# Kernel tuning notes

Hardware: AMD Instinct MI355X
Metric: run time of the kernel (lower is better)

Reference implementation:

```python
import jax, jax.numpy as jnp
import numpy as np

N_NODES = 50000      # nodes
N_EDGES = 800000     # directed edges (avg degree 16)
HIDDEN = 128
F_IN = 11            # QM9 num_node_features
NUM_CLASSES = 19     # QM9 num targets
NUM_GRAPHS = 2048


def _glorot(key, fan_in, fan_out):
    lim = np.sqrt(6.0 / (fan_in + fan_out)).astype(np.float32)
    return jax.random.uniform(key, (fan_in, fan_out), jnp.float32, -lim, lim)


def setup_inputs() -> dict:
    key = jax.random.key(0)
    ks = jax.random.split(key, 8)
    x = jax.random.normal(ks[0], (N_NODES, F_IN), jnp.float32)
    edge_index = jax.random.randint(ks[1], (2, N_EDGES), 0, N_NODES, dtype=jnp.int64)
    batch = jnp.sort(jax.random.randint(ks[2], (N_NODES,), 0, NUM_GRAPHS, dtype=jnp.int64))
    W1 = _glorot(ks[3], F_IN, HIDDEN); b1 = jnp.zeros((HIDDEN,), jnp.float32)
    W2 = _glorot(ks[4], HIDDEN, HIDDEN); b2 = jnp.zeros((HIDDEN,), jnp.float32)
    W3 = _glorot(ks[5], HIDDEN, HIDDEN); b3 = jnp.zeros((HIDDEN,), jnp.float32)
    Wl = _glorot(ks[6], HIDDEN, NUM_CLASSES); bl = jnp.zeros((NUM_CLASSES,), jnp.float32)
    return dict(x=x, edge_index=edge_index, batch=batch,
                W1=W1, b1=b1, W2=W2, b2=b2, W3=W3, b3=b3, Wl=Wl, bl=bl)


def gcn_conv(x, src, dst, W, b, n):
    """PyG GCNConv: x' = D^-1/2 (A + I) D^-1/2 (x W) + b, degrees include self-loops."""
    h = x @ W                                                      # [n, out]
    deg = jax.ops.segment_sum(jnp.ones_like(dst, h.dtype), dst, num_segments=n) + 1.0
    dinv = jax.lax.rsqrt(deg)                                      # [n]
    norm = dinv[src] * dinv[dst]                                   # [E]
    agg = jax.ops.segment_sum(h[src] * norm[:, None], dst, num_segments=n)
    agg = agg + h * (dinv * dinv)[:, None]                         # self-loop term
    return agg + b


def reference(x, edge_index, batch, W1, b1, W2, b2, W3, b3, Wl, bl):
    src, dst = edge_index[0], edge_index[1]
    h = jax.nn.relu(gcn_conv(x, src, dst, W1, b1, N_NODES))
    h = jax.nn.relu(gcn_conv(h, src, dst, W2, b2, N_NODES))
    h = gcn_conv(h, src, dst, W3, b3, N_NODES)
    # global_mean_pool over graph ids
    sums = jax.ops.segment_sum(h, batch, num_segments=NUM_GRAPHS)
    cnt = jax.ops.segment_sum(jnp.ones((N_NODES,), h.dtype), batch, num_segments=NUM_GRAPHS)
    pooled = sums / jnp.maximum(cnt, 1.0)[:, None]                 # [G, H]
    # dropout is identity in eval mode
    return pooled @ Wl + bl                                        # [G, NUM_CLASSES]
```

## Files before the change

kernel.cpp:

```cpp
#include <hip/hip_runtime.h>
#include <hip/hip_bf16.h>
#include <hip/hip_fp16.h>


#define HIDDEN 128
#define F_IN 11
#define NCLS 19
#define NBITS 8
#define NB 256
#define RNODES 256
#define EPB 4096
#define OUTL_CAP 5376
#define WST 136

typedef _Float16 half8 __attribute__((ext_vector_type(8)));
typedef _Float16 half2v __attribute__((ext_vector_type(2)));
typedef float floatx4 __attribute__((ext_vector_type(4)));

#define MIXFMA4(A, UX, UY, DV) \
    asm("v_fma_mix_f32 %0, %4, %5, %0 op_sel_hi:[1,0,0]\n\t" \
        "v_fma_mix_f32 %1, %4, %5, %1 op_sel:[1,0,0] op_sel_hi:[1,0,0]\n\t" \
        "v_fma_mix_f32 %2, %6, %5, %2 op_sel_hi:[1,0,0]\n\t" \
        "v_fma_mix_f32 %3, %6, %5, %3 op_sel:[1,0,0] op_sel_hi:[1,0,0]" \
        : "+v"(A.x), "+v"(A.y), "+v"(A.z), "+v"(A.w) \
        : "v"(UX), "v"(DV), "v"(UY))

#define MIXFMA2(AX, AY, UU, DV) \
    asm("v_fma_mix_f32 %0, %2, %3, %0 op_sel_hi:[1,0,0]\n\t" \
        "v_fma_mix_f32 %1, %2, %3, %1 op_sel:[1,0,0] op_sel_hi:[1,0,0]" \
        : "+v"(AX), "+v"(AY) : "v"(UU), "v"(DV))

#define MIXFMA1(AX, HU, DV) \
    asm("v_fma_mix_f32 %0, %1, %2, %0 op_sel_hi:[1,0,0]" \
        : "+v"(AX) : "v"(HU), "v"(DV))

#define DOT2(ACC, UA, UB) \
    ACC = __builtin_amdgcn_fdot2(__builtin_bit_cast(half2v, UA), \
                                 __builtin_bit_cast(half2v, UB), ACC, false)


__global__ __launch_bounds__(1024) void scatter_kernel(
        const int* __restrict__ src, const int* __restrict__ dst,
        int* __restrict__ bcur, unsigned int* __restrict__ bents,
        int E, int cap, int nSB,
        const float* __restrict__ W3, const float* __restrict__ Wl,
        const float* __restrict__ b3, __half* __restrict__ W3lTh,
        float* __restrict__ b3l, const float* __restrict__ W2,
        __half* __restrict__ W2Th) {
    __shared__ int hist[NB];
    __shared__ int binoff[NB];
    __shared__ int runrel[NB];
    __shared__ unsigned int ebuf[EPB];
    __shared__ unsigned short binOf[EPB];
    __shared__ int cw[4];
    int tid = threadIdx.x, lane = tid & 63, w = tid >> 6;

    if (blockIdx.x >= nSB) {
        int xb = blockIdx.x - nSB;
        if (xb < 3) {
            float* Wls = (float*)ebuf;
            for (int i = tid; i < HIDDEN * NCLS; i += 1024) Wls[i] = Wl[i];
            __syncthreads();
            int o = xb * 1024 + tid;
            if (o < HIDDEN * NCLS) {
                int i = o / NCLS, j = o % NCLS;
                float acc = 0.f;
#pragma unroll 8
                for (int k = 0; k < HIDDEN; ++k) acc += W3[i * HIDDEN + k] * Wls[k * NCLS + j];
                W3lTh[j * WST + i] = __float2half(acc);
            }
            if (xb == 2 && tid >= 1000 && tid < 1000 + NCLS) {
                int j = tid - 1000;
                float acc = 0.f;
#pragma unroll 8
                for (int k = 0; k < HIDDEN; ++k) acc += b3[k] * Wls[k * NCLS + j];
                b3l[j] = acc;
            }
        } else {
            int base = (xb - 3) * 4096;
#pragma unroll
            for (int r = 0; r < 4; ++r) {
                int idx = base + tid + 1024 * r;
                int k = idx >> 7, nn2 = idx & 127;
                W2Th[nn2 * HIDDEN + k] = __float2half(W2[idx]);
            }
        }
        return;
    }

    int base = blockIdx.x * EPB;
    int cnt = min(EPB, E - base);
    if (tid < NB) hist[tid] = 0;
    __syncthreads();
    unsigned int pk[4];
    int rk[4];
#pragma unroll
    for (int j = 0; j < 4; ++j) {
        int idx = tid + 1024 * j;
        if (idx < cnt) {
            int e = base + idx;
            int s = src[e], d = dst[e];
            pk[j] = (unsigned int)s | ((unsigned int)d << 16);
            int bin = d >> NBITS;
            int r = atomicAdd(&hist[bin], 1);
            rk[j] = r | (bin << 16);
        } else rk[j] = -1;
    }
    __syncthreads();
    if (tid < NB) {
        int v = hist[tid], xv = v;
#pragma unroll
        for (int d = 1; d < 64; d <<= 1) {
            int t = __shfl_up(xv, d, 64);
            if (lane >= d) xv += t;
        }
        if (lane == 63) cw[w] = xv;
        binoff[tid] = xv - v;
        runrel[tid] = v ? atomicAdd(&bcur[tid], v) : 0;
    }
    __syncthreads();
    if (tid < NB) {
        int waveoff = 0;
        for (int wi = 0; wi < w; ++wi) waveoff += cw[wi];
        binoff[tid] += waveoff;
    }
    __syncthreads();
#pragma unroll
    for (int j = 0; j < 4; ++j) {
        if (rk[j] >= 0) {
            int bin = rk[j] >> 16, r = rk[j] & 0xFFFF;
            int pos = binoff[bin] + r;
            ebuf[pos] = pk[j];
            binOf[pos] = (unsigned short)bin;
        }
    }
    __syncthreads();
    for (int i = tid; i < cnt; i += 1024) {
        int bin = binOf[i];
        int rel = runrel[bin] + (i - binoff[bin]);
        if (rel < cap)
            bents[bin * cap + rel] = ebuf[i];
    }
}

__global__ __launch_bounds__(1024) void build_kernel(
        const unsigned int* __restrict__ bents, const int* __restrict__ bcur,
        const float* __restrict__ x, const int* __restrict__ batch,
        int2* __restrict__ begend, unsigned short* __restrict__ csr16,
        float* __restrict__ dinv, float* __restrict__ gcnt,
        __half* __restrict__ x16h, int n, int cap, int rst) {
    __shared__ int counts[RNODES];
    __shared__ int lcur[RNODES];
    __shared__ unsigned short outl[OUTL_CAP];
    __shared__ int wsums[4];
    int tid = threadIdx.x;
    int lane = tid & 63, w = tid >> 6;
    int b = blockIdx.x;
    int base = b << NBITS;
    int nn = min(RNODES, n - base);
    int ebase = b * cap;
    int ecnt = min(bcur[b], cap);
    int st = b * rst;
    if (tid < RNODES) counts[tid] = 0;
    __syncthreads();
    for (int e = tid; e < ecnt; e += 1024)
        atomicAdd(&counts[(bents[ebase + e] >> 16) - base], 1);
    __syncthreads();
    int v = 0, xv = 0;
    if (tid < RNODES) {
        v = (tid < nn) ? counts[tid] + 1 : 0;
        xv = v;
#pragma unroll
        for (int d = 1; d < 64; d <<= 1) {
            int t = __shfl_up(xv, d, 64);
            if (lane >= d) xv += t;
        }
        if (lane == 63) wsums[w] = xv;
    }
    __syncthreads();
    if (tid < nn) {
        int waveoff = 0;
        for (int wi = 0; wi < w; ++wi) waveoff += wsums[wi];
        int excl = waveoff + xv - v;
        lcur[tid] = excl + 1;
        outl[excl] = (unsigned short)(base + tid);
        begend[base + tid] = make_int2(st + excl, st + excl + v);
        atomicAdd(&gcnt[batch[base + tid]], 1.0f);
    }
    __syncthreads();
    for (int e = tid; e < ecnt; e += 1024) {
        unsigned int pk = bents[ebase + e];
        int i = (int)(pk >> 16) - base;
        int r = atomicAdd(&lcur[i], 1);
        outl[r] = (unsigned short)(pk & 0xFFFFu);
    }
    __syncthreads();
    int total = ecnt + nn;
    for (int i = tid; i < total; i += 1024)
        csr16[st + i] = outl[i];
    for (int idx = tid; idx < nn * 16; idx += 1024) {
        int i = idx >> 4, j = idx & 15;
        float di = 1.0f / sqrtf((float)(counts[i] + 1));
        if (j == 0) dinv[base + i] = di;
        float xv2 = (j < F_IN) ? x[(long)(base + i) * F_IN + j] * di : 0.f;
        x16h[(long)(base + i) * 16 + j] = __float2half(xv2);
    }
}


__global__ __launch_bounds__(1024) void agg16_gemm_kernel(
        const __half* __restrict__ x16h, const int2* __restrict__ begend,
        const unsigned short* __restrict__ csr16,
        const float* __restrict__ dinv, const float* __restrict__ W1,
        const float* __restrict__ b1, __half* __restrict__ h1h, int n) {
    __shared__ float2 W1s[F_IN][64];
    __shared__ float2 bs[64];
    int tid = threadIdx.x;
    if (tid < 352) ((float4*)W1s)[tid] = ((const float4*)W1)[tid];
    if (tid >= 960) bs[tid - 960] = make_float2(b1[2 * (tid - 960)], b1[2 * (tid - 960) + 1]);
    __syncthreads();
    int node = (int)(((long)blockIdx.x * blockDim.x + tid) >> 6);
    int lane = tid & 63;
    if (node >= n) return;
    int grp = lane >> 4, f = lane & 15;
    float di = dinv[node];
    int2 be = begend[node];
    int beg = be.x, end = be.y;
    int deg = end - beg;
    int idxv = (lane < deg) ? (int)csr16[beg + lane] : 0;
    int lim = (deg > 64) ? beg + 64 : end;
    const unsigned short* x16u = (const unsigned short*)x16h;
    float acc = 0.f;
    int eb = beg;
    for (; eb + 16 <= lim; eb += 16) {
        int off = eb - beg;
        int s[4]; unsigned int v[4];
#pragma unroll
        for (int j = 0; j < 4; ++j) s[j] = __shfl(idxv, off + grp + 4 * j);
#pragma unroll
        for (int j = 0; j < 4; ++j) v[j] = x16u[(long)s[j] * 16 + f];
#pragma unroll
        for (int j = 0; j < 4; ++j) MIXFMA1(acc, v[j], di);
    }
    if (eb + 8 <= lim) {
        int off = eb - beg;
        int s0 = __shfl(idxv, off + grp), s1 = __shfl(idxv, off + grp + 4);
        unsigned int v0 = x16u[(long)s0 * 16 + f], v1 = x16u[(long)s1 * 16 + f];
        MIXFMA1(acc, v0, di);
        MIXFMA1(acc, v1, di);
        eb += 8;
    }
#pragma unroll
    for (int r = 0; r < 2; ++r) {
        int e = eb + grp + 4 * r;
        int s = __shfl(idxv, (e - beg) & 63);
        if (e < lim) {
            unsigned int v = x16u[(long)s * 16 + f];
            MIXFMA1(acc, v, di);
        }
    }
    for (int e = lim + grp; e < end; e += 4) {
        unsigned int v = x16u[(long)csr16[e] * 16 + f];
        MIXFMA1(acc, v, di);
    }
    acc += __shfl_down(acc, 32);
    acc += __shfl_down(acc, 16);
    float z = acc;
    float2 o = bs[lane];
#pragma unroll
    for (int k = 0; k < F_IN; ++k) {
        float zk = __shfl(z, k);
        float2 w = W1s[k][lane];
        o.x += zk * w.x;
        o.y += zk * w.y;
    }
    __half2 h = __floats2half2_rn(fmaxf(o.x, 0.f), fmaxf(o.y, 0.f));
    ((__half2*)h1h)[(long)node * 64 + lane] = h;
}


__global__ __launch_bounds__(256) void gemm_mfma_kernel(
        const __half* __restrict__ h1h, const __half* __restrict__ W2Th,
        const float* __restrict__ dinv, __half* __restrict__ hsh, int n) {
    __shared__ _Float16 W2T[128 * 136];
    __shared__ _Float16 outs[64 * 136];
    int tid = threadIdx.x;
    for (int i = tid; i < 128 * 16; i += 256) {
        int r = i >> 4, q = i & 15;
        *(uint4*)&W2T[r * 136 + q * 8] = ((const uint4*)W2Th)[r * 16 + q];
    }
    int base = blockIdx.x * 64;
    int lane = tid & 63, wid = tid >> 6;
    int l15 = lane & 15, quad = lane >> 4;
    int arow = base + wid * 16 + l15;
    if (arow >= n) arow = n - 1;
    const _Float16* Aptr = (const _Float16*)h1h + (size_t)arow * 128;
    floatx4 acc[8];
#pragma unroll
    for (int t = 0; t < 8; ++t) acc[t] = (floatx4){0.f, 0.f, 0.f, 0.f};
    __syncthreads();
#pragma unroll
    for (int c = 0; c < 4; ++c) {
        half8 a = *(const half8*)(Aptr + c * 32 + quad * 8);
#pragma unroll
        for (int t = 0; t < 8; ++t) {
            half8 b = *(const half8*)(&W2T[(t * 16 + l15) * 136 + c * 32 + quad * 8]);
            acc[t] = __builtin_amdgcn_mfma_f32_16x16x32_f16(a, b, acc[t], 0, 0, 0);
        }
    }
    float dv[4];
#pragma unroll
    for (int r = 0; r < 4; ++r) {
        int nd = base + wid * 16 + quad * 4 + r;
        dv[r] = dinv[(nd < n) ? nd : 0];
    }
#pragma unroll
    for (int t = 0; t < 8; ++t)
#pragma unroll
        for (int r = 0; r < 4; ++r)
            outs[(wid * 16 + quad * 4 + r) * 136 + t * 16 + l15] = (_Float16)(acc[t][r] * dv[r]);
    __syncthreads();
    for (int i = tid; i < 64 * 16; i += 256) {
        int ln = i >> 4, qq = i & 15;
        long nd = base + ln;
        if (nd < n) {
            uint4 u = *(uint4*)&outs[ln * 136 + qq * 8];
            ((uint4*)hsh)[nd * 16 + qq] = u;
        }
    }
}


__global__ __launch_bounds__(1024) void agg128h_y_kernel(
        const __half* __restrict__ hsh, const int2* __restrict__ begend,
        const unsigned short* __restrict__ csr16, const float* __restrict__ dinv,
        const float* __restrict__ bias, const __half* __restrict__ W3lTh,
        __half* __restrict__ ys, int n) {
    __shared__ _Float16 Ws[32 * WST];
    __shared__ _Float16 hs[16][HIDDEN];
    int tid = threadIdx.x;
    if (tid < 544) ((float4*)Ws)[tid] = ((const float4*)W3lTh)[tid];
    __syncthreads();
    int node = (int)(((long)blockIdx.x * blockDim.x + tid) >> 6);
    if (node >= n) return;
    int lane = tid & 63, w = tid >> 6;
    int grp = lane >> 5, q = lane & 31;
    float di = dinv[node];
    int2 be = begend[node];
    int beg = be.x, end = be.y;
    int deg = end - beg;
    int idxv = (lane < deg) ? (int)csr16[beg + lane] : 0;
    int lim = (deg > 64) ? beg + 64 : end;
    float4 acc = make_float4(0.f, 0.f, 0.f, 0.f);
    int eb = beg;
    for (; eb + 16 <= lim; eb += 16) {
        int off = eb - beg;
        int s[8]; uint2 u[8];
#pragma unroll
        for (int j = 0; j < 8; ++j) s[j] = __shfl(idxv, off + grp + 2 * j);
#pragma unroll
        for (int j = 0; j < 8; ++j) u[j] = ((const uint2*)hsh)[(long)s[j] * 32 + q];
#pragma unroll
        for (int j = 0; j < 8; ++j) MIXFMA4(acc, u[j].x, u[j].y, di);
    }
    if (eb + 8 <= lim) {
        int off = eb - beg;
        int s[4]; uint2 u[4];
#pragma unroll
        for (int j = 0; j < 4; ++j) s[j] = __shfl(idxv, off + grp + 2 * j);
#pragma unroll
        for (int j = 0; j < 4; ++j) u[j] = ((const uint2*)hsh)[(long)s[j] * 32 + q];
#pragma unroll
        for (int j = 0; j < 4; ++j) MIXFMA4(acc, u[j].x, u[j].y, di);
        eb += 8;
    }
#pragma unroll
    for (int r = 0; r < 4; ++r) {
        int e = eb + grp + 2 * r;
        int s = __shfl(idxv, (e - beg) & 63);
        if (e < lim) {
            uint2 u = ((const uint2*)hsh)[(long)s * 32 + q];
            MIXFMA4(acc, u.x, u.y, di);
        }
    }
    for (int e = lim + grp; e < end; e += 2) {
        uint2 u = ((const uint2*)hsh)[(long)csr16[e] * 32 + q];
        MIXFMA4(acc, u.x, u.y, di);
    }
    acc.x += __shfl_down(acc.x, 32);
    acc.y += __shfl_down(acc.y, 32);
    acc.z += __shfl_down(acc.z, 32);
    acc.w += __shfl_down(acc.w, 32);
    if (grp == 0) {
        float4 b = ((const float4*)bias)[q];
        __half2 p01 = __floats2half2_rn(fmaxf(acc.x + b.x, 0.f), fmaxf(acc.y + b.y, 0.f));
        __half2 p23 = __floats2half2_rn(fmaxf(acc.z + b.z, 0.f), fmaxf(acc.w + b.w, 0.f));
        uint2 hv = make_uint2(*(unsigned int*)&p01, *(unsigned int*)&p23);
        *(uint2*)&hs[w][q * 4] = hv;
    }
    asm volatile("s_waitcnt lgkmcnt(0)" ::: "memory");
    float yacc = 0.f;
    int kbase = grp * 64;
    if (q < NCLS) {
#pragma unroll
        for (int kk = 0; kk < 8; ++kk) {
            int k0 = kbase + kk * 8;
            uint4 ua = *(uint4*)&hs[w][k0];
            uint4 ub = *(uint4*)&Ws[q * WST + k0];
            DOT2(yacc, ua.x, ub.x);
            DOT2(yacc, ua.y, ub.y);
            DOT2(yacc, ua.z, ub.z);
            DOT2(yacc, ua.w, ub.w);
        }
    }
    yacc += __shfl_down(yacc, 32);
    if (lane < NCLS)
        ys[(long)node * 32 + lane] = __float2half(yacc * di);
}


__global__ __launch_bounds__(1024) void agg24h_pool_kernel(
        const __half* __restrict__ ys, const int2* __restrict__ begend,
        const unsigned short* __restrict__ csr16, const float* __restrict__ dinv,
        const int* __restrict__ batch, float* __restrict__ pool, int n) {
    __shared__ float pg[32 * 24];
    __shared__ int g0s;
    int tid = threadIdx.x;
    long nbase = (long)blockIdx.x * 16;
    if (tid == 0) g0s = batch[nbase < n ? nbase : (n - 1)];
    if (tid < 32 * 24) pg[tid] = 0.f;
    __syncthreads();
    int g0 = g0s;
    int node = (int)(nbase + (tid >> 6));
    int lane = tid & 63;
    bool active = node < n;
    int grp = lane >> 4, f = lane & 15;
    float2 acc = {0.f, 0.f};
    if (active) {
        float sc = dinv[node];
        int2 be = begend[node];
        int beg = be.x, end = be.y;
        int deg = end - beg;
        int idxv = (lane < deg) ? (int)csr16[beg + lane] : 0;
        int lim = (deg > 64) ? beg + 64 : end;
        int eb = beg;
        for (; eb + 32 <= lim; eb += 32) {
            int off = eb - beg;
            int s[8]; unsigned int u[8];
#pragma unroll
            for (int j = 0; j < 8; ++j) s[j] = __shfl(idxv, off + grp + 4 * j);
#pragma unroll
            for (int j = 0; j < 8; ++j) u[j] = ((const unsigned int*)ys)[(long)s[j] * 16 + f];
#pragma unroll
            for (int j = 0; j < 8; ++j) MIXFMA2(acc.x, acc.y, u[j], sc);
        }
        if (eb + 16 <= lim) {
            int off = eb - beg;
            int s[4]; unsigned int u[4];
#pragma unroll
            for (int j = 0; j < 4; ++j) s[j] = __shfl(idxv, off + grp + 4 * j);
#pragma unroll
            for (int j = 0; j < 4; ++j) u[j] = ((const unsigned int*)ys)[(long)s[j] * 16 + f];
#pragma unroll
            for (int j = 0; j < 4; ++j) MIXFMA2(acc.x, acc.y, u[j], sc);
            eb += 16;
        }
#pragma unroll
        for (int r = 0; r < 4; ++r) {
            int e = eb + grp + 4 * r;
            int s = __shfl(idxv, (e - beg) & 63);
            if (e < lim) {
                unsigned int u = ((const unsigned int*)ys)[(long)s * 16 + f];
                MIXFMA2(acc.x, acc.y, u, sc);
            }
        }
        for (int e = lim + grp; e < end; e += 4) {
            unsigned int u = ((const unsigned int*)ys)[(long)csr16[e] * 16 + f];
            MIXFMA2(acc.x, acc.y, u, sc);
        }
        acc.x += __shfl_down(acc.x, 32);
        acc.y += __shfl_down(acc.y, 32);
        acc.x += __shfl_down(acc.x, 16);
        acc.y += __shfl_down(acc.y, 16);
        if (lane < 16) {
            int g = batch[node];
            int slot = g - g0;
            int c0 = 2 * f;
            if (slot < 32) {
                if (c0 < NCLS) atomicAdd(&pg[slot * 24 + c0], acc.x);
                if (c0 + 1 < NCLS) atomicAdd(&pg[slot * 24 + c0 + 1], acc.y);
            } else {
                if (c0 < NCLS) atomicAdd(&pool[(long)g * 24 + c0], acc.x);
                if (c0 + 1 < NCLS) atomicAdd(&pool[(long)g * 24 + c0 + 1], acc.y);
            }
        }
    }
    __syncthreads();
    if (tid < 32 * 24) {
        float v = pg[tid];
        if (v != 0.f) {
            int slot = tid / 24, c = tid - slot * 24;
            atomicAdd(&pool[(long)(g0 + slot) * 24 + c], v);
        }
    }
}

__global__ void final_kernel(const float* __restrict__ pool, const float* __restrict__ cnt,
                             const float* __restrict__ b3l, const float* __restrict__ bl,
                             float* __restrict__ out, int G) {
    int i = blockIdx.x * blockDim.x + threadIdx.x;
    if (i >= G * NCLS) return;
    int g = i / NCLS, j = i % NCLS;
    float c = cnt[g];
    out[i] = (c > 0.f) ? pool[(long)g * 24 + j] / c + b3l[j] + bl[j] : bl[j];
}


static inline size_t align256(size_t x) { return (x + 255) & ~(size_t)255; }

extern "C" void kernel_launch(void* const* d_in, const int* in_sizes, int n_in,
                              void* d_out, int out_size, void* d_ws, size_t ws_size,
                              hipStream_t stream) {
    const float* x    = (const float*)d_in[0];
    const int*   ei   = (const int*)d_in[1];
    const int*   batch= (const int*)d_in[2];
    const float* W1   = (const float*)d_in[3];
    const float* b1   = (const float*)d_in[4];
    const float* W2   = (const float*)d_in[5];
    const float* b2   = (const float*)d_in[6];
    const float* W3   = (const float*)d_in[7];
    const float* b3   = (const float*)d_in[8];
    const float* Wl   = (const float*)d_in[9];
    const float* bl   = (const float*)d_in[10];
    float* out = (float*)d_out;

    const int N = in_sizes[0] / F_IN;
    const int E = in_sizes[1] / 2;
    const int G = out_size / NCLS;
    const int* src = ei;
    const int* dst = ei + E;
    const int nSB = (E + EPB - 1) / EPB;
    const int nBK = (N + RNODES - 1) / RNODES;
    int cap = (int)((long long)E * RNODES / N) + 768;
    if (cap + RNODES > OUTL_CAP) cap = OUTL_CAP - RNODES;
    const int rst = cap + RNODES;

    char* p = (char*)d_ws;
    size_t off = 0;
    unsigned int*   bents  = (unsigned int*)(p + off);   off = align256(off + (size_t)NB * cap * 4);
    unsigned short* csr16  = (unsigned short*)(p + off); off = align256(off + (size_t)NB * rst * 2);
    int2*           begend = (int2*)(p + off);           off = align256(off + (size_t)N * 8);
    float*          dinv   = (float*)(p + off);          off = align256(off + (size_t)N * 4);
    __half*         x16h   = (__half*)(p + off);         off = align256(off + (size_t)N * 16 * 2);
    __half*         h1h    = (__half*)(p + off);         off = align256(off + (size_t)N * HIDDEN * 2);
    __half*         hsh    = (__half*)(p + off);         off = align256(off + (size_t)N * HIDDEN * 2);
    __half*         y32h   = (__half*)(p + off);         off = align256(off + (size_t)N * 32 * 2);
    __half*         W2Th   = (__half*)(p + off);         off = align256(off + (size_t)HIDDEN * HIDDEN * 2);
    __half*         W3lTh  = (__half*)(p + off);         off = align256(off + (size_t)32 * WST * 2);
    float*          b3l    = (float*)(p + off);          off = align256(off + (size_t)NCLS * 4);
    float*          pool   = (float*)(p + off);
    float*          gcnt   = pool + (size_t)G * 24;
    int*            bcur   = (int*)(pool + (size_t)G * 25);
    off = align256(off + (size_t)G * 25 * 4 + NB * 4);
    (void)ws_size; (void)n_in;

    hipMemsetAsync(pool, 0, (size_t)G * 25 * 4 + NB * 4, stream);

    scatter_kernel<<<nSB + 7, 1024, 0, stream>>>(src, dst, bcur, bents, E, cap, nSB,
                                                 W3, Wl, b3, W3lTh, b3l, W2, W2Th);
    build_kernel<<<nBK, 1024, 0, stream>>>(bents, bcur, x, batch, begend, csr16,
                                           dinv, gcnt, x16h, N, cap, rst);

    const int aggBlocks16 = (N + 15) / 16;

    agg16_gemm_kernel<<<aggBlocks16, 1024, 0, stream>>>(x16h, begend, csr16, dinv, W1, b1, h1h, N);

    gemm_mfma_kernel<<<(N + 63) / 64, 256, 0, stream>>>(h1h, W2Th, dinv, hsh, N);

    agg128h_y_kernel<<<aggBlocks16, 1024, 0, stream>>>(hsh, begend, csr16, dinv, b2, W3lTh, y32h, N);

    agg24h_pool_kernel<<<aggBlocks16, 1024, 0, stream>>>(y32h, begend, csr16, dinv, batch, pool, N);
    final_kernel<<<(G * NCLS + 255) / 256, 256, 0, stream>>>(pool, gcnt, b3l, bl, out, G);
}
```

Measured before the change: 201.2 us.

## Replace binned CSR build with fixed-capacity per-node adjacency via global atomics

```diff
diff --git a/kernel.cpp b/kernel.cpp
--- a/kernel.cpp
+++ b/kernel.cpp
@@ -6,11 +6,8 @@
 #define HIDDEN 128
 #define F_IN 11
 #define NCLS 19
-#define NBITS 8
-#define NB 256
-#define RNODES 256
 #define EPB 4096
-#define OUTL_CAP 5376
+#define CAPA 64
 #define WST 136
 
 typedef _Float16 half8 __attribute__((ext_vector_type(8)));
@@ -41,24 +38,18 @@
 
 __global__ __launch_bounds__(1024) void scatter_kernel(
         const int* __restrict__ src, const int* __restrict__ dst,
-        int* __restrict__ bcur, unsigned int* __restrict__ bents,
-        int E, int cap, int nSB,
+        int* __restrict__ deg, unsigned short* __restrict__ adj,
+        int E, int nSB,
         const float* __restrict__ W3, const float* __restrict__ Wl,
         const float* __restrict__ b3, __half* __restrict__ W3lTh,
         float* __restrict__ b3l, const float* __restrict__ W2,
         __half* __restrict__ W2Th) {
-    __shared__ int hist[NB];
-    __shared__ int binoff[NB];
-    __shared__ int runrel[NB];
-    __shared__ unsigned int ebuf[EPB];
-    __shared__ unsigned short binOf[EPB];
-    __shared__ int cw[4];
-    int tid = threadIdx.x, lane = tid & 63, w = tid >> 6;
+    __shared__ float Wls[HIDDEN * NCLS];
+    int tid = threadIdx.x;
 
     if (blockIdx.x >= nSB) {
         int xb = blockIdx.x - nSB;
         if (xb < 3) {
-            float* Wls = (float*)ebuf;
             for (int i = tid; i < HIDDEN * NCLS; i += 1024) Wls[i] = Wl[i];
             __syncthreads();
             int o = xb * 1024 + tid;
@@ -90,127 +81,40 @@
 
     int base = blockIdx.x * EPB;
     int cnt = min(EPB, E - base);
-    if (tid < NB) hist[tid] = 0;
-    __syncthreads();
-    unsigned int pk[4];
-    int rk[4];
 #pragma unroll
     for (int j = 0; j < 4; ++j) {
         int idx = tid + 1024 * j;
         if (idx < cnt) {
             int e = base + idx;
             int s = src[e], d = dst[e];
-            pk[j] = (unsigned int)s | ((unsigned int)d << 16);
-            int bin = d >> NBITS;
-            int r = atomicAdd(&hist[bin], 1);
-            rk[j] = r | (bin << 16);
-        } else rk[j] = -1;
-    }
-    __syncthreads();
-    if (tid < NB) {
-        int v = hist[tid], xv = v;
-#pragma unroll
-        for (int d = 1; d < 64; d <<= 1) {
-            int t = __shfl_up(xv, d, 64);
-            if (lane >= d) xv += t;
-        }
-        if (lane == 63) cw[w] = xv;
-        binoff[tid] = xv - v;
-        runrel[tid] = v ? atomicAdd(&bcur[tid], v) : 0;
-    }
-    __syncthreads();
-    if (tid < NB) {
-        int waveoff = 0;
-        for (int wi = 0; wi < w; ++wi) waveoff += cw[wi];
-        binoff[tid] += waveoff;
-    }
-    __syncthreads();
-#pragma unroll
-    for (int j = 0; j < 4; ++j) {
-        if (rk[j] >= 0) {
-            int bin = rk[j] >> 16, r = rk[j] & 0xFFFF;
-            int pos = binoff[bin] + r;
-            ebuf[pos] = pk[j];
-            binOf[pos] = (unsigned short)bin;
-        }
-    }
-    __syncthreads();
-    for (int i = tid; i < cnt; i += 1024) {
-        int bin = binOf[i];
-        int rel = runrel[bin] + (i - binoff[bin]);
-        if (rel < cap)
-            bents[bin * cap + rel] = ebuf[i];
-    }
-}
+            int slot = atomicAdd(&deg[d], 1);
+            if (slot < CAPA)
+                adj[(long)d * CAPA + slot] = (unsigned short)s;
+        }
+    }
+}
+
 
 __global__ __launch_bounds__(1024) void build_kernel(
-        const unsigned int* __restrict__ bents, const int* __restrict__ bcur,
-        const float* __restrict__ x, const int* __restrict__ batch,
-        int2* __restrict__ begend, unsigned short* __restrict__ csr16,
-        float* __restrict__ dinv, float* __restrict__ gcnt,
-        __half* __restrict__ x16h, int n, int cap, int rst) {
-    __shared__ int counts[RNODES];
-    __shared__ int lcur[RNODES];
-    __shared__ unsigned short outl[OUTL_CAP];
-    __shared__ int wsums[4];
-    int tid = threadIdx.x;
-    int lane = tid & 63, w = tid >> 6;
-    int b = blockIdx.x;
-    int base = b << NBITS;
-    int nn = min(RNODES, n - base);
-    int ebase = b * cap;
-    int ecnt = min(bcur[b], cap);
-    int st = b * rst;
-    if (tid < RNODES) counts[tid] = 0;
-    __syncthreads();
-    for (int e = tid; e < ecnt; e += 1024)
-        atomicAdd(&counts[(bents[ebase + e] >> 16) - base], 1);
-    __syncthreads();
-    int v = 0, xv = 0;
-    if (tid < RNODES) {
-        v = (tid < nn) ? counts[tid] + 1 : 0;
-        xv = v;
-#pragma unroll
-        for (int d = 1; d < 64; d <<= 1) {
-            int t = __shfl_up(xv, d, 64);
-            if (lane >= d) xv += t;
-        }
-        if (lane == 63) wsums[w] = xv;
-    }
-    __syncthreads();
-    if (tid < nn) {
-        int waveoff = 0;
-        for (int wi = 0; wi < w; ++wi) waveoff += wsums[wi];
-        int excl = waveoff + xv - v;
-        lcur[tid] = excl + 1;
-        outl[excl] = (unsigned short)(base + tid);
-        begend[base + tid] = make_int2(st + excl, st + excl + v);
-        atomicAdd(&gcnt[batch[base + tid]], 1.0f);
-    }
-    __syncthreads();
-    for (int e = tid; e < ecnt; e += 1024) {
-        unsigned int pk = bents[ebase + e];
-        int i = (int)(pk >> 16) - base;
-        int r = atomicAdd(&lcur[i], 1);
-        outl[r] = (unsigned short)(pk & 0xFFFFu);
-    }
-    __syncthreads();
-    int total = ecnt + nn;
-    for (int i = tid; i < total; i += 1024)
-        csr16[st + i] = outl[i];
-    for (int idx = tid; idx < nn * 16; idx += 1024) {
-        int i = idx >> 4, j = idx & 15;
-        float di = 1.0f / sqrtf((float)(counts[i] + 1));
-        if (j == 0) dinv[base + i] = di;
-        float xv2 = (j < F_IN) ? x[(long)(base + i) * F_IN + j] * di : 0.f;
-        x16h[(long)(base + i) * 16 + j] = __float2half(xv2);
-    }
+        const int* __restrict__ deg, const float* __restrict__ x,
+        const int* __restrict__ batch, float* __restrict__ dinv,
+        float* __restrict__ gcnt, __half* __restrict__ x16h, int n) {
+    long idx = (long)blockIdx.x * 1024 + threadIdx.x;
+    if (idx >= (long)n * 16) return;
+    int i = (int)(idx >> 4), j = (int)(idx & 15);
+    float di = 1.0f / sqrtf((float)(deg[i] + 1));
+    if (j == 0) {
+        dinv[i] = di;
+        atomicAdd(&gcnt[batch[i]], 1.0f);
+    }
+    float xv = (j < F_IN) ? x[(long)i * F_IN + j] * di : 0.f;
+    x16h[(long)i * 16 + j] = __float2half(xv);
 }
 
 
 __global__ __launch_bounds__(1024) void agg16_gemm_kernel(
-        const __half* __restrict__ x16h, const int2* __restrict__ begend,
-        const unsigned short* __restrict__ csr16,
+        const __half* __restrict__ x16h, const unsigned short* __restrict__ adj,
+        const int* __restrict__ deg,
         const float* __restrict__ dinv, const float* __restrict__ W1,
         const float* __restrict__ b1, __half* __restrict__ h1h, int n) {
     __shared__ float2 W1s[F_IN][64];
@@ -224,27 +128,26 @@
     if (node >= n) return;
     int grp = lane >> 4, f = lane & 15;
     float di = dinv[node];
-    int2 be = begend[node];
-    int beg = be.x, end = be.y;
-    int deg = end - beg;
-    int idxv = (lane < deg) ? (int)csr16[beg + lane] : 0;
-    int lim = (deg > 64) ? beg + 64 : end;
+    int dn = min(deg[node], CAPA);
+    int idxv = (lane < dn) ? (int)adj[(long)node * CAPA + lane] : 0;
     const unsigned short* x16u = (const unsigned short*)x16h;
     float acc = 0.f;
-    int eb = beg;
-    for (; eb + 16 <= lim; eb += 16) {
-        int off = eb - beg;
+    if (grp == 0) {
+        unsigned int v = x16u[(long)node * 16 + f];
+        MIXFMA1(acc, v, di);
+    }
+    int eb = 0;
+    for (; eb + 16 <= dn; eb += 16) {
         int s[4]; unsigned int v[4];
 #pragma unroll
-        for (int j = 0; j < 4; ++j) s[j] = __shfl(idxv, off + grp + 4 * j);
+        for (int j = 0; j < 4; ++j) s[j] = __shfl(idxv, eb + grp + 4 * j);
 #pragma unroll
         for (int j = 0; j < 4; ++j) v[j] = x16u[(long)s[j] * 16 + f];
 #pragma unroll
         for (int j = 0; j < 4; ++j) MIXFMA1(acc, v[j], di);
     }
-    if (eb + 8 <= lim) {
-        int off = eb - beg;
-        int s0 = __shfl(idxv, off + grp), s1 = __shfl(idxv, off + grp + 4);
+    if (eb + 8 <= dn) {
+        int s0 = __shfl(idxv, eb + grp), s1 = __shfl(idxv, eb + grp + 4);
         unsigned int v0 = x16u[(long)s0 * 16 + f], v1 = x16u[(long)s1 * 16 + f];
         MIXFMA1(acc, v0, di);
         MIXFMA1(acc, v1, di);
@@ -253,15 +156,11 @@
 #pragma unroll
     for (int r = 0; r < 2; ++r) {
         int e = eb + grp + 4 * r;
-        int s = __shfl(idxv, (e - beg) & 63);
-        if (e < lim) {
+        int s = __shfl(idxv, e & 63);
+        if (e < dn) {
             unsigned int v = x16u[(long)s * 16 + f];
             MIXFMA1(acc, v, di);
         }
-    }
-    for (int e = lim + grp; e < end; e += 4) {
-        unsigned int v = x16u[(long)csr16[e] * 16 + f];
-        MIXFMA1(acc, v, di);
     }
     acc += __shfl_down(acc, 32);
     acc += __shfl_down(acc, 16);
@@ -332,8 +231,8 @@
 
 
 __global__ __launch_bounds__(1024) void agg128h_y_kernel(
-        const __half* __restrict__ hsh, const int2* __restrict__ begend,
-        const unsigned short* __restrict__ csr16, const float* __restrict__ dinv,
+        const __half* __restrict__ hsh, const unsigned short* __restrict__ adj,
+        const int* __restrict__ deg, const float* __restrict__ dinv,
         const float* __restrict__ bias, const __half* __restrict__ W3lTh,
         __half* __restrict__ ys, int n) {
     __shared__ _Float16 Ws[32 * WST];
@@ -346,28 +245,27 @@
     int lane = tid & 63, w = tid >> 6;
     int grp = lane >> 5, q = lane & 31;
     float di = dinv[node];
-    int2 be = begend[node];
-    int beg = be.x, end = be.y;
-    int deg = end - beg;
-    int idxv = (lane < deg) ? (int)csr16[beg + lane] : 0;
-    int lim = (deg > 64) ? beg + 64 : end;
+    int dn = min(deg[node], CAPA);
+    int idxv = (lane < dn) ? (int)adj[(long)node * CAPA + lane] : 0;
     float4 acc = make_float4(0.f, 0.f, 0.f, 0.f);
-    int eb = beg;
-    for (; eb + 16 <= lim; eb += 16) {
-        int off = eb - beg;
+    if (grp == 0) {
+        uint2 u = ((const uint2*)hsh)[(long)node * 32 + q];
+        MIXFMA4(acc, u.x, u.y, di);
+    }
+    int eb = 0;
+    for (; eb + 16 <= dn; eb += 16) {
         int s[8]; uint2 u[8];
 #pragma unroll
-        for (int j = 0; j < 8; ++j) s[j] = __shfl(idxv, off + grp + 2 * j);
+        for (int j = 0; j < 8; ++j) s[j] = __shfl(idxv, eb + grp + 2 * j);
 #pragma unroll
         for (int j = 0; j < 8; ++j) u[j] = ((const uint2*)hsh)[(long)s[j] * 32 + q];
 #pragma unroll
         for (int j = 0; j < 8; ++j) MIXFMA4(acc, u[j].x, u[j].y, di);
     }
-    if (eb + 8 <= lim) {
-        int off = eb - beg;
+    if (eb + 8 <= dn) {
         int s[4]; uint2 u[4];
 #pragma unroll
-        for (int j = 0; j < 4; ++j) s[j] = __shfl(idxv, off + grp + 2 * j);
+        for (int j = 0; j < 4; ++j) s[j] = __shfl(idxv, eb + grp + 2 * j);
 #pragma unroll
         for (int j = 0; j < 4; ++j) u[j] = ((const uint2*)hsh)[(long)s[j] * 32 + q];
 #pragma unroll
@@ -377,15 +275,11 @@
 #pragma unroll
     for (int r = 0; r < 4; ++r) {
         int e = eb + grp + 2 * r;
-        int s = __shfl(idxv, (e - beg) & 63);
-        if (e < lim) {
+        int s = __shfl(idxv, e & 63);
+        if (e < dn) {
             uint2 u = ((const uint2*)hsh)[(long)s * 32 + q];
             MIXFMA4(acc, u.x, u.y, di);
         }
-    }
-    for (int e = lim + grp; e < end; e += 2) {
-        uint2 u = ((const uint2*)hsh)[(long)csr16[e] * 32 + q];
-        MIXFMA4(acc, u.x, u.y, di);
     }
     acc.x += __shfl_down(acc.x, 32);
     acc.y += __shfl_down(acc.y, 32);
@@ -420,8 +314,8 @@
 
 
 __global__ __launch_bounds__(1024) void agg24h_pool_kernel(
-        const __half* __restrict__ ys, const int2* __restrict__ begend,
-        const unsigned short* __restrict__ csr16, const float* __restrict__ dinv,
+        const __half* __restrict__ ys, const unsigned short* __restrict__ adj,
+        const int* __restrict__ deg, const float* __restrict__ dinv,
         const int* __restrict__ batch, float* __restrict__ pool, int n) {
     __shared__ float pg[32 * 24];
     __shared__ int g0s;
@@ -438,27 +332,26 @@
     float2 acc = {0.f, 0.f};
     if (active) {
         float sc = dinv[node];
-        int2 be = begend[node];
-        int beg = be.x, end = be.y;
-        int deg = end - beg;
-        int idxv = (lane < deg) ? (int)csr16[beg + lane] : 0;
-        int lim = (deg > 64) ? beg + 64 : end;
-        int eb = beg;
-        for (; eb + 32 <= lim; eb += 32) {
-            int off = eb - beg;
+        int dn = min(deg[node], CAPA);
+        int idxv = (lane < dn) ? (int)adj[(long)node * CAPA + lane] : 0;
+        if (grp == 0) {
+            unsigned int u = ((const unsigned int*)ys)[(long)node * 16 + f];
+            MIXFMA2(acc.x, acc.y, u, sc);
+        }
+        int eb = 0;
+        for (; eb + 32 <= dn; eb += 32) {
             int s[8]; unsigned int u[8];
 #pragma unroll
-            for (int j = 0; j < 8; ++j) s[j] = __shfl(idxv, off + grp + 4 * j);
+            for (int j = 0; j < 8; ++j) s[j] = __shfl(idxv, eb + grp + 4 * j);
 #pragma unroll
             for (int j = 0; j < 8; ++j) u[j] = ((const unsigned int*)ys)[(long)s[j] * 16 + f];
 #pragma unroll
             for (int j = 0; j < 8; ++j) MIXFMA2(acc.x, acc.y, u[j], sc);
         }
-        if (eb + 16 <= lim) {
-            int off = eb - beg;
+        if (eb + 16 <= dn) {
             int s[4]; unsigned int u[4];
 #pragma unroll
-            for (int j = 0; j < 4; ++j) s[j] = __shfl(idxv, off + grp + 4 * j);
+            for (int j = 0; j < 4; ++j) s[j] = __shfl(idxv, eb + grp + 4 * j);
 #pragma unroll
             for (int j = 0; j < 4; ++j) u[j] = ((const unsigned int*)ys)[(long)s[j] * 16 + f];
 #pragma unroll
@@ -468,15 +361,11 @@
 #pragma unroll
         for (int r = 0; r < 4; ++r) {
             int e = eb + grp + 4 * r;
-            int s = __shfl(idxv, (e - beg) & 63);
-            if (e < lim) {
+            int s = __shfl(idxv, e & 63);
+            if (e < dn) {
                 unsigned int u = ((const unsigned int*)ys)[(long)s * 16 + f];
                 MIXFMA2(acc.x, acc.y, u, sc);
             }
-        }
-        for (int e = lim + grp; e < end; e += 4) {
-            unsigned int u = ((const unsigned int*)ys)[(long)csr16[e] * 16 + f];
-            MIXFMA2(acc.x, acc.y, u, sc);
         }
         acc.x += __shfl_down(acc.x, 32);
         acc.y += __shfl_down(acc.y, 32);
@@ -540,16 +429,10 @@
     const int* src = ei;
     const int* dst = ei + E;
     const int nSB = (E + EPB - 1) / EPB;
-    const int nBK = (N + RNODES - 1) / RNODES;
-    int cap = (int)((long long)E * RNODES / N) + 768;
-    if (cap + RNODES > OUTL_CAP) cap = OUTL_CAP - RNODES;
-    const int rst = cap + RNODES;
 
     char* p = (char*)d_ws;
     size_t off = 0;
-    unsigned int*   bents  = (unsigned int*)(p + off);   off = align256(off + (size_t)NB * cap * 4);
-    unsigned short* csr16  = (unsigned short*)(p + off); off = align256(off + (size_t)NB * rst * 2);
-    int2*           begend = (int2*)(p + off);           off = align256(off + (size_t)N * 8);
+    unsigned short* adj    = (unsigned short*)(p + off); off = align256(off + (size_t)N * CAPA * 2);
     float*          dinv   = (float*)(p + off);          off = align256(off + (size_t)N * 4);
     __half*         x16h   = (__half*)(p + off);         off = align256(off + (size_t)N * 16 * 2);
     __half*         h1h    = (__half*)(p + off);         off = align256(off + (size_t)N * HIDDEN * 2);
@@ -560,25 +443,25 @@
     float*          b3l    = (float*)(p + off);          off = align256(off + (size_t)NCLS * 4);
     float*          pool   = (float*)(p + off);
     float*          gcnt   = pool + (size_t)G * 24;
-    int*            bcur   = (int*)(pool + (size_t)G * 25);
-    off = align256(off + (size_t)G * 25 * 4 + NB * 4);
+    int*            deg    = (int*)(pool + (size_t)G * 25);
+    off = align256(off + (size_t)G * 25 * 4 + (size_t)N * 4);
     (void)ws_size; (void)n_in;
 
-    hipMemsetAsync(pool, 0, (size_t)G * 25 * 4 + NB * 4, stream);
-
-    scatter_kernel<<<nSB + 7, 1024, 0, stream>>>(src, dst, bcur, bents, E, cap, nSB,
+    hipMemsetAsync(pool, 0, (size_t)G * 25 * 4 + (size_t)N * 4, stream);
+
+    scatter_kernel<<<nSB + 7, 1024, 0, stream>>>(src, dst, deg, adj, E, nSB,
                                                  W3, Wl, b3, W3lTh, b3l, W2, W2Th);
-    build_kernel<<<nBK, 1024, 0, stream>>>(bents, bcur, x, batch, begend, csr16,
-                                           dinv, gcnt, x16h, N, cap, rst);
+    build_kernel<<<(int)(((long)N * 16 + 1023) / 1024), 1024, 0, stream>>>(
+        deg, x, batch, dinv, gcnt, x16h, N);
 
     const int aggBlocks16 = (N + 15) / 16;
 
-    agg16_gemm_kernel<<<aggBlocks16, 1024, 0, stream>>>(x16h, begend, csr16, dinv, W1, b1, h1h, N);
+    agg16_gemm_kernel<<<aggBlocks16, 1024, 0, stream>>>(x16h, adj, deg, dinv, W1, b1, h1h, N);
 
     gemm_mfma_kernel<<<(N + 63) / 64, 256, 0, stream>>>(h1h, W2Th, dinv, hsh, N);
 
-    agg128h_y_kernel<<<aggBlocks16, 1024, 0, stream>>>(hsh, begend, csr16, dinv, b2, W3lTh, y32h, N);
-
-    agg24h_pool_kernel<<<aggBlocks16, 1024, 0, stream>>>(y32h, begend, csr16, dinv, batch, pool, N);
+    agg128h_y_kernel<<<aggBlocks16, 1024, 0, stream>>>(hsh, adj, deg, dinv, b2, W3lTh, y32h, N);
+
+    agg24h_pool_kernel<<<aggBlocks16, 1024, 0, stream>>>(y32h, adj, deg, dinv, batch, pool, N);
     final_kernel<<<(G * NCLS + 255) / 256, 256, 0, stream>>>(pool, gcnt, b3l, bl, out, G);
 }
```

New measurement: 250.5 us. 1.24x slower.
